# Kernel tuning notes

Measured on AMD Instinct MI355X. Metric: run time of the kernel, lower is better.

The kernel has to match this reference:

```python
import jax, jax.numpy as jnp
import numpy as np
from functools import partial

B, N, T = 4, 10000, 128
E = 160000
H, C = 4, 64            # heads, out_channels per head
GAT_DIM = H * C         # 256
NEG_SLOPE = 0.2


def conv1d(x, w, b):
    # x: (M, Cin, L), w: (Cout, Cin, K), 'same' padding (pad=1 for k=3)
    y = jax.lax.conv_general_dilated(x, w, window_strides=(1,), padding=[(1, 1)],
                                     dimension_numbers=('NCH', 'OIH', 'NCH'))
    return y + b[None, :, None]


def maxpool2(x):
    # kernel=2, stride=2 over last axis
    return jax.lax.reduce_window(x, -jnp.inf, jax.lax.max,
                                 (1, 1, 2), (1, 1, 2), 'VALID')


def gat_layer_single(x, src, dst, W, att_s, att_d, bias):
    # x: (N, Fin); PyG GATConv with concat=True, self-loops already appended to src/dst
    n = x.shape[0]
    xl = (x @ W).reshape(n, H, C)                       # (N, H, C)
    a_s = jnp.sum(xl * att_s[None], axis=-1)            # (N, H)
    a_d = jnp.sum(xl * att_d[None], axis=-1)            # (N, H)
    e = jax.nn.leaky_relu(a_s[src] + a_d[dst], NEG_SLOPE)  # (E', H)
    emax = jax.ops.segment_max(e, dst, num_segments=n)     # (N, H)
    ex = jnp.exp(e - emax[dst])
    denom = jax.ops.segment_sum(ex, dst, num_segments=n)   # (N, H)
    alpha = ex / (denom[dst] + 1e-16)                       # (E', H)
    msg = xl[src] * alpha[..., None]                        # (E', H, C)
    out = jax.ops.segment_sum(msg, dst, num_segments=n)     # (N, H, C)
    return out.reshape(n, H * C) + bias


def setup_inputs() -> dict:
    key = jax.random.key(0)
    ks = jax.random.split(key, 24)
    rn = lambda k, sh, fan: jax.random.normal(k, sh, jnp.float32) / np.sqrt(fan)
    inp = {
        'x': jax.random.normal(ks[0], (B, N, T), jnp.float32),
        'edge_index': jax.random.randint(ks[1], (2, E), 0, N, jnp.int64),
        # temporal conv
        'cw1': rn(ks[2], (32, 1, 3), 3), 'cb1': jnp.zeros((32,), jnp.float32),
        'cw2': rn(ks[3], (64, 32, 3), 96), 'cb2': jnp.zeros((64,), jnp.float32),
        # GAT layer 0 (in=64)
        'W0': rn(ks[4], (64, GAT_DIM), 64), 'as0': rn(ks[5], (H, C), C), 'ad0': rn(ks[6], (H, C), C),
        'b0': jnp.zeros((GAT_DIM,), jnp.float32),
        # GAT layer 1 (in=256)
        'W1': rn(ks[7], (GAT_DIM, GAT_DIM), GAT_DIM), 'as1': rn(ks[8], (H, C), C), 'ad1': rn(ks[9], (H, C), C),
        'b1': jnp.zeros((GAT_DIM,), jnp.float32),
        # classification head 256->128->2
        'Wc1': rn(ks[10], (GAT_DIM, 128), GAT_DIM), 'bc1': jnp.zeros((128,), jnp.float32),
        'Wc2': rn(ks[11], (128, 2), 128), 'bc2': jnp.zeros((2,), jnp.float32),
        # attribution head 256->64->1
        'Wa1': rn(ks[12], (GAT_DIM, 64), GAT_DIM), 'ba1': jnp.zeros((64,), jnp.float32),
        'Wa2': rn(ks[13], (64, 1), 64), 'ba2': jnp.zeros((1,), jnp.float32),
    }
    return inp


def reference(x, edge_index, cw1, cb1, cw2, cb2, W0, as0, ad0, b0, W1, as1, ad1, b1,
              Wc1, bc1, Wc2, bc2, Wa1, ba1, Wa2, ba2):
    b, n, t = x.shape
    # ---- temporal conv over all B*N node signals ----
    xf = x.reshape(b * n, 1, t)
    h = jax.nn.relu(conv1d(xf, cw1, cb1))            # (BN, 32, T)
    h = maxpool2(h)                                  # (BN, 32, T//2)
    h = jax.nn.relu(conv1d(h, cw2, cb2))             # (BN, 64, T//2)
    feat = jnp.mean(h, axis=-1).reshape(b, n, 64)    # adaptive_avg_pool1d(1)
    # ---- GAT stack (self-loops appended, PyG default) ----
    src0, dst0 = edge_index[0], edge_index[1]
    loops = jnp.arange(n, dtype=src0.dtype)
    src = jnp.concatenate([src0, loops])
    dst = jnp.concatenate([dst0, loops])
    gat0 = jax.vmap(partial(gat_layer_single, src=src, dst=dst, W=W0, att_s=as0, att_d=ad0, bias=b0))
    gat1 = jax.vmap(partial(gat_layer_single, src=src, dst=dst, W=W1, att_s=as1, att_d=ad1, bias=b1))
    g = jax.nn.relu(gat0(feat))                      # (B, N, 256); dropout = identity (eval)
    g = jax.nn.relu(gat1(g))                         # (B, N, 256)
    # ---- heads ----
    pooled = jnp.mean(g, axis=1)                     # (B, 256)
    logits = jax.nn.relu(pooled @ Wc1 + bc1) @ Wc2 + bc2          # (B, 2)
    attr = jax.nn.sigmoid(jax.nn.relu(g @ Wa1 + ba1) @ Wa2 + ba2)  # (B, N, 1)
    return logits, attr[..., 0]
```

## Files before the change

kernel.cpp:

```cpp
#include <hip/hip_runtime.h>
#include <hip/hip_bf16.h>
#include <math.h>

typedef __hip_bfloat16 bf16;
typedef unsigned short u16;
typedef unsigned int u32;
typedef __attribute__((ext_vector_type(8))) short short8;
typedef __attribute__((ext_vector_type(4))) float f32x4;
typedef __attribute__((ext_vector_type(2))) float f32x2;

#define BATCH 4
#define NNODE 10000
#define TLEN 128
#define NEDGE 160000
#define GDIM 256
#define NHEAD 4

#define S_CW1 0
#define S_CB1 96
#define S_CB2 128
#define S_AS0 192
#define S_AD0 448
#define S_B0  704
#define S_AS1 960
#define S_AD1 1216
#define S_B1  1472
#define S_BC1 1728
#define S_WC2 1856
#define S_BC2 2112
#define S_BA1 2114
#define S_WA2 2178
#define S_BA2 2242
#define S_TOTAL 2243

__device__ __forceinline__ float prelu(float v) { return fmaxf(v, 0.f); }
__device__ __forceinline__ u16 f2b(float f) {
    union { float f; u32 u; } v; v.f = f;
    u32 r = v.u + 0x7FFF + ((v.u >> 16) & 1);
    return (u16)(r >> 16);
}
__device__ __forceinline__ float u2f(u16 u) {
    union { u32 u; float f; } v; v.u = ((u32)u) << 16;
    return v.f;
}
__device__ __forceinline__ float ldw(const void* p, int off, bool isbf) {
    return isbf ? u2f(((const u16*)p)[off]) : ((const float*)p)[off];
}

__device__ __forceinline__ bool probe_x_bf16(const void* xsrc) {
    int lane = threadIdx.x & 63;
    u16 h = ((const u16*)xsrc)[2 * lane];
    int e = (h >> 7) & 0xFF;
    unsigned long long m = __ballot(e >= 117 && e <= 130);
    return __popcll(m) >= 32;
}
__device__ __forceinline__ bool probe_ei64(const int* ei) {
    int lane = threadIdx.x & 63;
    int v = ei[2 * lane + 1];
    unsigned long long m = __ballot(v == 0);
    return __popcll(m) >= 56;
}

struct WPtrs { const void* p[20]; };

#define PRE_TBLK 665
__global__ __launch_bounds__(256) void k_pre(WPtrs wp, const void* __restrict__ xsrc,
        const int* __restrict__ ei, float* __restrict__ wbuf,
        u16* __restrict__ cw2r, u16* __restrict__ W0t, u16* __restrict__ W1t,
        u16* __restrict__ Wa1t, int* __restrict__ counts) {
    bool isbf = probe_x_bf16(xsrc);
    int b = blockIdx.x;
    if (b >= PRE_TBLK) {
        const int C2[16] = {0,96,128,192,448,704,960,1216,1472,1728,1856,2112,
                            2114,2178,2242,2243};
        const int SRC[15] = {0,1,3,5,6,7,9,10,11,13,14,15,17,18,19};
        int i = (b - PRE_TBLK) * 256 + threadIdx.x;
        if (i >= S_TOTAL) return;
        int j = 14;
        for (int t = 0; t < 15; ++t) { if (i < C2[t + 1]) { j = t; break; } }
        wbuf[i] = ldw(wp.p[SRC[j]], i - C2[j], isbf);
        return;
    }
    int i = b * 256 + threadIdx.x;
    if (i < 6144) {
        int c2 = i / 96, k = i - c2 * 96, s = k >> 5, ci = k & 31;
        cw2r[i] = f2b(ldw(wp.p[2], c2 * 96 + ci * 3 + s, isbf));
    }
    if (i < 16384) {
        int k = i >> 8, c = i & 255;
        W0t[c * 64 + k] = f2b(ldw(wp.p[4], k * 256 + c, isbf));
        int ka = i >> 6, ca = i & 63;
        Wa1t[ca * 256 + ka] = f2b(ldw(wp.p[16], ka * 64 + ca, isbf));
    }
    if (i < 65536) {
        int k = i >> 8, c = i & 255;
        W1t[c * 256 + k] = f2b(ldw(wp.p[8], k * 256 + c, isbf));
    }
    if (i < NEDGE + NNODE) {
        bool ei64 = probe_ei64(ei);
        int dst;
        if (i < NEDGE) dst = ei64 ? ei[2 * (NEDGE + i)] : ei[NEDGE + i];
        else dst = i - NEDGE;
        if (dst >= 0 && dst < NNODE) atomicAdd(&counts[dst], 1);
    }
}

__global__ __launch_bounds__(1024) void k_scan(const int* __restrict__ counts,
        int* __restrict__ cur, int* __restrict__ row_ptr) {
    __shared__ int buf[1024];
    int t = threadIdx.x;
    int base = t * 10;
    int c[10];
    int s = 0;
    #pragma unroll
    for (int i = 0; i < 10; ++i) {
        int idx = base + i;
        c[i] = (idx < NNODE) ? counts[idx] : 0;
        s += c[i];
    }
    buf[t] = s;
    __syncthreads();
    for (int off = 1; off < 1024; off <<= 1) {
        int v = (t >= off) ? buf[t - off] : 0;
        __syncthreads();
        buf[t] += v;
        __syncthreads();
    }
    int run = buf[t] - s;
    #pragma unroll
    for (int i = 0; i < 10; ++i) {
        int idx = base + i;
        if (idx < NNODE) {
            cur[idx] = run;
            run += c[i];
            row_ptr[idx + 1] = run;
        }
    }
    if (t == 0) row_ptr[0] = 0;
}

#define HSTR 40
#define FSTR 72
#define NPW 4
#define FILL_BLK 665
__global__ __launch_bounds__(256) void k_conv(const void* __restrict__ xsrc,
        const float* __restrict__ wbuf, const u16* __restrict__ cw2r,
        const u16* __restrict__ W0t, u16* __restrict__ featb,
        u16* __restrict__ xlb, float* __restrict__ a_s, float* __restrict__ a_d,
        const int* __restrict__ ei, int* __restrict__ cur, int* __restrict__ col_src) {
    __shared__ __align__(16) float xs[4][132];
    __shared__ float w1s[96], b1s[32], b2s[64];
    __shared__ __align__(16) u16 hb[4][66 * HSTR];
    __shared__ __align__(16) u16 fs[16][FSTR];

    bool isbf = probe_x_bf16(xsrc);
    int tid = threadIdx.x;
    int wave = tid >> 6, lane = tid & 63;
    int node0 = blockIdx.x * (4 * NPW);

    int m = lane & 15, q = lane >> 4;
    short8 bfr[4][3];
    #pragma unroll
    for (int nt = 0; nt < 4; ++nt)
        #pragma unroll
        for (int sh = 0; sh < 3; ++sh)
            bfr[nt][sh] = *(const short8*)&cw2r[(nt * 16 + m) * 96 + sh * 32 + q * 8];

    if (tid < 96) w1s[tid] = wbuf[S_CW1 + tid];
    if (tid < 32) b1s[tid] = wbuf[S_CB1 + tid];
    if (tid < 64) b2s[tid] = wbuf[S_CB2 + tid];
    if (tid < 8) xs[tid >> 1][(tid & 1) ? 129 : 0] = 0.f;
    if (tid < 64) {
        int w = tid >> 4, idx = tid & 15;
        *(u32*)&hb[w][2 * idx] = 0;
        *(u32*)&hb[w][65 * HSTR + 2 * idx] = 0;
    }
    __syncthreads();

    float* xsw = xs[wave];
    u16* hw = &hb[wave][0];

    int d = m, uu = q;
    float wa0 = w1s[6 * d + 0], wa1 = w1s[6 * d + 1], wa2 = w1s[6 * d + 2];
    float wb0 = w1s[6 * d + 3], wb1 = w1s[6 * d + 4], wb2 = w1s[6 * d + 5];
    float ba = b1s[2 * d], bb = b1s[2 * d + 1];
    float b2vv[4];
    #pragma unroll
    for (int nt = 0; nt < 4; ++nt) b2vv[nt] = b2s[nt * 16 + m];

    int node = node0 + wave;
    u32 plo = 0; float2 pf = {0.f, 0.f};
    if (isbf) plo = ((const u32*)xsrc)[(size_t)node * 64 + lane];
    else      pf  = ((const float2*)xsrc)[(size_t)node * 64 + lane];

    for (int j = 0; j < NPW; ++j) {
        if (isbf) {
            xsw[1 + 2 * lane] = u2f((u16)(plo & 0xFFFF));
            xsw[2 + 2 * lane] = u2f((u16)(plo >> 16));
        } else {
            xsw[1 + 2 * lane] = pf.x;
            xsw[2 + 2 * lane] = pf.y;
        }
        if (j + 1 < NPW) {
            int nxt = node + 4;
            if (isbf) plo = ((const u32*)xsrc)[(size_t)nxt * 64 + lane];
            else      pf  = ((const float2*)xsrc)[(size_t)nxt * 64 + lane];
        }

        #pragma unroll
        for (int it = 0; it < 16; ++it) {
            int u = uu + 4 * it;
            int t0 = 2 * u;
            float2 xa = *(const float2*)&xsw[t0];
            float2 xb = *(const float2*)&xsw[t0 + 2];
            float x0 = xa.x, x1 = xa.y, x2 = xb.x, x3 = xb.y;
            f32x2 A = {x0, x1}, Bv = {x1, x2}, Cv = {x2, x3};
            f32x2 va = {ba, ba}; va += wa0 * A; va += wa1 * Bv; va += wa2 * Cv;
            f32x2 vb = {bb, bb}; vb += wb0 * A; vb += wb1 * Bv; vb += wb2 * Cv;
            float ha = fmaxf(fmaxf(va.x, va.y), 0.f);
            float hb2 = fmaxf(fmaxf(vb.x, vb.y), 0.f);
            __hip_bfloat162 hp2 = __float22bfloat162_rn(make_float2(ha, hb2));
            u32 pack; __builtin_memcpy(&pack, &hp2, 4);
            *(u32*)&hw[(u + 1) * HSTR + 2 * d] = pack;
        }

        float pc0 = 0.f, pc1 = 0.f, pc2 = 0.f, pc3 = 0.f;
        #pragma unroll
        for (int mt = 0; mt < 4; ++mt) {
            const u16* hr = &hw[(mt * 16 + m) * HSTR + q * 8];
            short8 a0 = *(const short8*)&hr[0 * HSTR];
            short8 a1 = *(const short8*)&hr[1 * HSTR];
            short8 a2 = *(const short8*)&hr[2 * HSTR];
            f32x4 c0 = {0.f,0.f,0.f,0.f}, c1 = {0.f,0.f,0.f,0.f};
            f32x4 c2 = {0.f,0.f,0.f,0.f}, c3 = {0.f,0.f,0.f,0.f};
            c0 = __builtin_amdgcn_mfma_f32_16x16x32_bf16(a0, bfr[0][0], c0, 0, 0, 0);
            c1 = __builtin_amdgcn_mfma_f32_16x16x32_bf16(a0, bfr[1][0], c1, 0, 0, 0);
            c2 = __builtin_amdgcn_mfma_f32_16x16x32_bf16(a0, bfr[2][0], c2, 0, 0, 0);
            c3 = __builtin_amdgcn_mfma_f32_16x16x32_bf16(a0, bfr[3][0], c3, 0, 0, 0);
            c0 = __builtin_amdgcn_mfma_f32_16x16x32_bf16(a1, bfr[0][1], c0, 0, 0, 0);
            c1 = __builtin_amdgcn_mfma_f32_16x16x32_bf16(a1, bfr[1][1], c1, 0, 0, 0);
            c2 = __builtin_amdgcn_mfma_f32_16x16x32_bf16(a1, bfr[2][1], c2, 0, 0, 0);
            c3 = __builtin_amdgcn_mfma_f32_16x16x32_bf16(a1, bfr[3][1], c3, 0, 0, 0);
            c0 = __builtin_amdgcn_mfma_f32_16x16x32_bf16(a2, bfr[0][2], c0, 0, 0, 0);
            c1 = __builtin_amdgcn_mfma_f32_16x16x32_bf16(a2, bfr[1][2], c1, 0, 0, 0);
            c2 = __builtin_amdgcn_mfma_f32_16x16x32_bf16(a2, bfr[2][2], c2, 0, 0, 0);
            c3 = __builtin_amdgcn_mfma_f32_16x16x32_bf16(a2, bfr[3][2], c3, 0, 0, 0);
            pc0 += prelu(c0[0] + b2vv[0]) + prelu(c0[1] + b2vv[0])
                 + prelu(c0[2] + b2vv[0]) + prelu(c0[3] + b2vv[0]);
            pc1 += prelu(c1[0] + b2vv[1]) + prelu(c1[1] + b2vv[1])
                 + prelu(c1[2] + b2vv[1]) + prelu(c1[3] + b2vv[1]);
            pc2 += prelu(c2[0] + b2vv[2]) + prelu(c2[1] + b2vv[2])
                 + prelu(c2[2] + b2vv[2]) + prelu(c2[3] + b2vv[2]);
            pc3 += prelu(c3[0] + b2vv[3]) + prelu(c3[1] + b2vv[3])
                 + prelu(c3[2] + b2vv[3]) + prelu(c3[3] + b2vv[3]);
        }
        pc0 += __shfl_xor(pc0, 16, 64); pc0 += __shfl_xor(pc0, 32, 64);
        pc1 += __shfl_xor(pc1, 16, 64); pc1 += __shfl_xor(pc1, 32, 64);
        pc2 += __shfl_xor(pc2, 16, 64); pc2 += __shfl_xor(pc2, 32, 64);
        pc3 += __shfl_xor(pc3, 16, 64); pc3 += __shfl_xor(pc3, 32, 64);
        float v = (q == 0) ? pc0 : (q == 1) ? pc1 : (q == 2) ? pc2 : pc3;
        u16 fv = f2b(v * (1.f / 64.f));
        if (node < 32) featb[(size_t)node * 64 + lane] = fv;
        fs[wave + 4 * j][lane] = fv;

        node += 4;
    }

    if (blockIdx.x < FILL_BLK) {
        bool ei64 = probe_ei64(ei);
        int e = blockIdx.x * 256 + tid;
        if (e < NEDGE + NNODE) {
            int src, dst;
            if (e < NEDGE) {
                if (ei64) { src = ei[2 * e]; dst = ei[2 * (NEDGE + e)]; }
                else      { src = ei[e];     dst = ei[NEDGE + e]; }
            } else {
                src = dst = e - NEDGE;
            }
            if (dst >= 0 && dst < NNODE) {
                int pos = atomicAdd(&cur[dst], 1);
                if (pos >= 0 && pos < NEDGE + NNODE) col_src[pos] = src;
            }
        }
    }

    __syncthreads();

    {
        f32x4 acc[4];
        #pragma unroll
        for (int ntl = 0; ntl < 4; ++ntl) acc[ntl] = {0.f, 0.f, 0.f, 0.f};
        #pragma unroll
        for (int kc = 0; kc < 64; kc += 32) {
            short8 a = *(const short8*)&fs[m][kc + q * 8];
            #pragma unroll
            for (int ntl = 0; ntl < 4; ++ntl) {
                int col0 = wave * 64 + ntl * 16;
                short8 bw = *(const short8*)&W0t[(size_t)(col0 + m) * 64 + kc + q * 8];
                acc[ntl] = __builtin_amdgcn_mfma_f32_16x16x32_bf16(a, bw, acc[ntl], 0, 0, 0);
            }
        }
        #pragma unroll
        for (int ntl = 0; ntl < 4; ++ntl) {
            #pragma unroll
            for (int r = 0; r < 4; ++r)
                xlb[(size_t)(node0 + q * 4 + r) * 256 + wave * 64 + ntl * 16 + m]
                    = f2b(acc[ntl][r]);
        }
        const float* asw_p = wbuf + S_AS0;
        const float* adw_p = wbuf + S_AD0;
        float sh_s[4] = {0, 0, 0, 0}, sh_d[4] = {0, 0, 0, 0};
        #pragma unroll
        for (int ntl = 0; ntl < 4; ++ntl) {
            float asw = asw_p[wave * 64 + ntl * 16 + m];
            float adw = adw_p[wave * 64 + ntl * 16 + m];
            #pragma unroll
            for (int r = 0; r < 4; ++r) {
                sh_s[r] += acc[ntl][r] * asw;
                sh_d[r] += acc[ntl][r] * adw;
            }
        }
        #pragma unroll
        for (int off = 1; off < 16; off <<= 1) {
            #pragma unroll
            for (int r = 0; r < 4; ++r) {
                sh_s[r] += __shfl_xor(sh_s[r], off, 64);
                sh_d[r] += __shfl_xor(sh_d[r], off, 64);
            }
        }
        if (m == 0) {
            int bb2 = node0 / NNODE;
            int nn0 = node0 - bb2 * NNODE;
            #pragma unroll
            for (int r = 0; r < 4; ++r) {
                int nn = nn0 + q * 4 + r;
                a_s[(size_t)nn * 16 + bb2 * 4 + wave] = sh_s[r];
                a_d[(size_t)nn * 16 + bb2 * 4 + wave] = sh_d[r];
            }
        }
    }
}

#define GSTR 264
__global__ __launch_bounds__(512) void k_agg_gemm(const u16* __restrict__ xlb,
        const float* __restrict__ a_s, const float* __restrict__ a_d,
        const int* __restrict__ row_ptr, const int* __restrict__ col_src,
        const float* __restrict__ bias, const u16* __restrict__ W1t,
        const float* __restrict__ wbuf, u16* __restrict__ outb,
        float* __restrict__ as_out, float* __restrict__ ad_out) {
    __shared__ __align__(16) u16 gt[16][GSTR];
    __shared__ float ps_s[8][16], ps_d[8][16];

    int tid = threadIdx.x;
    int wave = tid >> 6, lane = tid & 63;
    int dl = wave >> 1;
    int dst = __builtin_amdgcn_readfirstlane(blockIdx.x * 4 + dl);
    int bp = (wave & 1) * 2;
    int beg = __builtin_amdgcn_readfirstlane(row_ptr[dst]);
    int end = __builtin_amdgcn_readfirstlane(row_ptr[dst + 1]);

    int bl = lane >> 5;
    int s = lane & 31;
    int h = s >> 3;
    int b = bp + bl;
    int asoff = b * 4 + h;
    size_t rowb = (size_t)b * NNODE;
    float advh = a_d[(size_t)dst * 16 + asoff];

    float m = -INFINITY, l = 0.f;
    float acc[8];
    #pragma unroll
    for (int k = 0; k < 8; ++k) acc[k] = 0.f;

    int i = beg;
    int n0 = 0, n1 = 0, n2 = 0, n3 = 0;
    if (i + 4 <= end) {
        n0 = col_src[i]; n1 = col_src[i + 1];
        n2 = col_src[i + 2]; n3 = col_src[i + 3];
    }
    while (i + 4 <= end) {
        int s0 = min(max(n0, 0), NNODE - 1);
        int s1 = min(max(n1, 0), NNODE - 1);
        int s2 = min(max(n2, 0), NNODE - 1);
        int s3 = min(max(n3, 0), NNODE - 1);
        float a0 = a_s[(size_t)s0 * 16 + asoff];
        float a1 = a_s[(size_t)s1 * 16 + asoff];
        float a2 = a_s[(size_t)s2 * 16 + asoff];
        float a3 = a_s[(size_t)s3 * 16 + asoff];
        short8 x0 = *(const short8*)&xlb[(rowb + s0) * 256 + s * 8];
        short8 x1 = *(const short8*)&xlb[(rowb + s1) * 256 + s * 8];
        short8 x2 = *(const short8*)&xlb[(rowb + s2) * 256 + s * 8];
        short8 x3 = *(const short8*)&xlb[(rowb + s3) * 256 + s * 8];
        i += 4;
        if (i + 4 <= end) {
            n0 = col_src[i]; n1 = col_src[i + 1];
            n2 = col_src[i + 2]; n3 = col_src[i + 3];
        }
        float e0 = a0 + advh; e0 = (e0 >= 0.f) ? e0 : 0.2f * e0;
        float e1 = a1 + advh; e1 = (e1 >= 0.f) ? e1 : 0.2f * e1;
        float e2 = a2 + advh; e2 = (e2 >= 0.f) ? e2 : 0.2f * e2;
        float e3 = a3 + advh; e3 = (e3 >= 0.f) ? e3 : 0.2f * e3;
        float cmax = fmaxf(fmaxf(e0, e1), fmaxf(e2, e3));
        if (__any(cmax > m)) {
            float mn = fmaxf(m, cmax);
            float r = __expf(m - mn);
            m = mn;
            l *= r;
            #pragma unroll
            for (int k = 0; k < 8; ++k) acc[k] *= r;
        }
        float p0 = __expf(e0 - m); l += p0;
        #pragma unroll
        for (int k = 0; k < 8; ++k) acc[k] += p0 * u2f((u16)x0[k]);
        float p1 = __expf(e1 - m); l += p1;
        #pragma unroll
        for (int k = 0; k < 8; ++k) acc[k] += p1 * u2f((u16)x1[k]);
        float p2 = __expf(e2 - m); l += p2;
        #pragma unroll
        for (int k = 0; k < 8; ++k) acc[k] += p2 * u2f((u16)x2[k]);
        float p3 = __expf(e3 - m); l += p3;
        #pragma unroll
        for (int k = 0; k < 8; ++k) acc[k] += p3 * u2f((u16)x3[k]);
    }
    for (; i < end; ++i) {
        int s0 = min(max(col_src[i], 0), NNODE - 1);
        float a0 = a_s[(size_t)s0 * 16 + asoff];
        short8 x0 = *(const short8*)&xlb[(rowb + s0) * 256 + s * 8];
        float e0 = a0 + advh; e0 = (e0 >= 0.f) ? e0 : 0.2f * e0;
        if (__any(e0 > m)) {
            float mn = fmaxf(m, e0);
            float r = __expf(m - mn);
            m = mn;
            l *= r;
            #pragma unroll
            for (int k = 0; k < 8; ++k) acc[k] *= r;
        }
        float p0 = __expf(e0 - m); l += p0;
        #pragma unroll
        for (int k = 0; k < 8; ++k) acc[k] += p0 * u2f((u16)x0[k]);
    }

    float rl = 1.f / (l + 1e-16f);
    short8 o;
    #pragma unroll
    for (int k = 0; k < 8; ++k)
        o[k] = (short)f2b(prelu(acc[k] * rl + bias[s * 8 + k]));
    int grow = dl * 4 + b;
    *(short8*)&gt[grow][s * 8] = o;
    __syncthreads();

    int mm = lane & 15, q = lane >> 4;
    f32x4 ac2[2];
    ac2[0] = {0.f, 0.f, 0.f, 0.f};
    ac2[1] = {0.f, 0.f, 0.f, 0.f};
    for (int kc = 0; kc < 256; kc += 32) {
        short8 a = *(const short8*)&gt[mm][kc + q * 8];
        #pragma unroll
        for (int ntl = 0; ntl < 2; ++ntl) {
            short8 bw = *(const short8*)&W1t[(size_t)(wave * 32 + ntl * 16 + mm) * 256 + kc + q * 8];
            ac2[ntl] = __builtin_amdgcn_mfma_f32_16x16x32_bf16(a, bw, ac2[ntl], 0, 0, 0);
        }
    }
    int dbase = blockIdx.x * 4;
    #pragma unroll
    for (int ntl = 0; ntl < 2; ++ntl) {
        #pragma unroll
        for (int r = 0; r < 4; ++r)
            outb[((size_t)r * NNODE + dbase + q) * 256 + wave * 32 + ntl * 16 + mm]
                = f2b(ac2[ntl][r]);
    }
    float sh_s[4] = {0, 0, 0, 0}, sh_d[4] = {0, 0, 0, 0};
    #pragma unroll
    for (int ntl = 0; ntl < 2; ++ntl) {
        int col = wave * 32 + ntl * 16 + mm;
        float asw = wbuf[S_AS1 + col];
        float adw = wbuf[S_AD1 + col];
        #pragma unroll
        for (int r = 0; r < 4; ++r) {
            sh_s[r] += ac2[ntl][r] * asw;
            sh_d[r] += ac2[ntl][r] * adw;
        }
    }
    #pragma unroll
    for (int off = 1; off < 16; off <<= 1) {
        #pragma unroll
        for (int r = 0; r < 4; ++r) {
            sh_s[r] += __shfl_xor(sh_s[r], off, 64);
            sh_d[r] += __shfl_xor(sh_d[r], off, 64);
        }
    }
    if (mm == 0) {
        #pragma unroll
        for (int r = 0; r < 4; ++r) {
            ps_s[wave][q * 4 + r] = sh_s[r];
            ps_d[wave][q * 4 + r] = sh_d[r];
        }
    }
    __syncthreads();
    if (tid < 128) {
        int sd = tid >> 6, hh = (tid >> 4) & 3, row2 = tid & 15;
        int nn = dbase + (row2 >> 2), bb = row2 & 3;
        if (sd == 0)
            as_out[(size_t)nn * 16 + bb * 4 + hh] = ps_s[2 * hh][row2] + ps_s[2 * hh + 1][row2];
        else
            ad_out[(size_t)nn * 16 + bb * 4 + hh] = ps_d[2 * hh][row2] + ps_d[2 * hh + 1][row2];
    }
}

__global__ __launch_bounds__(512) void k_agg_attr(const u16* __restrict__ gb,
        const float* __restrict__ a_s, const float* __restrict__ a_d,
        const int* __restrict__ row_ptr, const int* __restrict__ col_src,
        const float* __restrict__ bias, const u16* __restrict__ Wa1t,
        const float* __restrict__ wbuf, u16* __restrict__ gdiag,
        float* __restrict__ out, float* __restrict__ pooled) {
    __shared__ __align__(16) u16 gt[16][GSTR];
    __shared__ float ps_a[4][16];

    int tid = threadIdx.x;
    int wave = tid >> 6, lane = tid & 63;
    int dl = wave >> 1;
    int dst = __builtin_amdgcn_readfirstlane(blockIdx.x * 4 + dl);
    int bp = (wave & 1) * 2;
    int beg = __builtin_amdgcn_readfirstlane(row_ptr[dst]);
    int end = __builtin_amdgcn_readfirstlane(row_ptr[dst + 1]);

    int bl = lane >> 5;
    int s = lane & 31;
    int h = s >> 3;
    int b = bp + bl;
    int asoff = b * 4 + h;
    size_t rowb = (size_t)b * NNODE;
    float advh = a_d[(size_t)dst * 16 + asoff];

    float m = -INFINITY, l = 0.f;
    float acc[8];
    #pragma unroll
    for (int k = 0; k < 8; ++k) acc[k] = 0.f;

    int i = beg;
    int n0 = 0, n1 = 0, n2 = 0, n3 = 0;
    if (i + 4 <= end) {
        n0 = col_src[i]; n1 = col_src[i + 1];
        n2 = col_src[i + 2]; n3 = col_src[i + 3];
    }
    while (i + 4 <= end) {
        int s0 = min(max(n0, 0), NNODE - 1);
        int s1 = min(max(n1, 0), NNODE - 1);
        int s2 = min(max(n2, 0), NNODE - 1);
        int s3 = min(max(n3, 0), NNODE - 1);
        float a0 = a_s[(size_t)s0 * 16 + asoff];
        float a1 = a_s[(size_t)s1 * 16 + asoff];
        float a2 = a_s[(size_t)s2 * 16 + asoff];
        float a3 = a_s[(size_t)s3 * 16 + asoff];
        short8 x0 = *(const short8*)&gb[(rowb + s0) * 256 + s * 8];
        short8 x1 = *(const short8*)&gb[(rowb + s1) * 256 + s * 8];
        short8 x2 = *(const short8*)&gb[(rowb + s2) * 256 + s * 8];
        short8 x3 = *(const short8*)&gb[(rowb + s3) * 256 + s * 8];
        i += 4;
        if (i + 4 <= end) {
            n0 = col_src[i]; n1 = col_src[i + 1];
            n2 = col_src[i + 2]; n3 = col_src[i + 3];
        }
        float e0 = a0 + advh; e0 = (e0 >= 0.f) ? e0 : 0.2f * e0;
        float e1 = a1 + advh; e1 = (e1 >= 0.f) ? e1 : 0.2f * e1;
        float e2 = a2 + advh; e2 = (e2 >= 0.f) ? e2 : 0.2f * e2;
        float e3 = a3 + advh; e3 = (e3 >= 0.f) ? e3 : 0.2f * e3;
        float cmax = fmaxf(fmaxf(e0, e1), fmaxf(e2, e3));
        if (__any(cmax > m)) {
            float mn = fmaxf(m, cmax);
            float r = __expf(m - mn);
            m = mn;
            l *= r;
            #pragma unroll
            for (int k = 0; k < 8; ++k) acc[k] *= r;
        }
        float p0 = __expf(e0 - m); l += p0;
        #pragma unroll
        for (int k = 0; k < 8; ++k) acc[k] += p0 * u2f((u16)x0[k]);
        float p1 = __expf(e1 - m); l += p1;
        #pragma unroll
        for (int k = 0; k < 8; ++k) acc[k] += p1 * u2f((u16)x1[k]);
        float p2 = __expf(e2 - m); l += p2;
        #pragma unroll
        for (int k = 0; k < 8; ++k) acc[k] += p2 * u2f((u16)x2[k]);
        float p3 = __expf(e3 - m); l += p3;
        #pragma unroll
        for (int k = 0; k < 8; ++k) acc[k] += p3 * u2f((u16)x3[k]);
    }
    for (; i < end; ++i) {
        int s0 = min(max(col_src[i], 0), NNODE - 1);
        float a0 = a_s[(size_t)s0 * 16 + asoff];
        short8 x0 = *(const short8*)&gb[(rowb + s0) * 256 + s * 8];
        float e0 = a0 + advh; e0 = (e0 >= 0.f) ? e0 : 0.2f * e0;
        if (__any(e0 > m)) {
            float mn = fmaxf(m, e0);
            float r = __expf(m - mn);
            m = mn;
            l *= r;
            #pragma unroll
            for (int k = 0; k < 8; ++k) acc[k] *= r;
        }
        float p0 = __expf(e0 - m); l += p0;
        #pragma unroll
        for (int k = 0; k < 8; ++k) acc[k] += p0 * u2f((u16)x0[k]);
    }

    float rl = 1.f / (l + 1e-16f);
    short8 o;
    #pragma unroll
    for (int k = 0; k < 8; ++k)
        o[k] = (short)f2b(prelu(acc[k] * rl + bias[s * 8 + k]));
    *(short8*)&gt[dl * 4 + b][s * 8] = o;
    if (b == 0 && dst < 8)
        *(short8*)&gdiag[(size_t)dst * 256 + s * 8] = o;
    __syncthreads();

    int dbase = blockIdx.x * 4;
    int mm = lane & 15, q = lane >> 4;
    if (wave < 4) {
        f32x4 ac2 = {0.f, 0.f, 0.f, 0.f};
        for (int kc = 0; kc < 256; kc += 32) {
            short8 a = *(const short8*)&gt[mm][kc + q * 8];
            short8 bw = *(const short8*)&Wa1t[(size_t)(wave * 16 + mm) * 256 + kc + q * 8];
            ac2 = __builtin_amdgcn_mfma_f32_16x16x32_bf16(a, bw, ac2, 0, 0, 0);
        }
        int col = wave * 16 + mm;
        float ba1v = wbuf[S_BA1 + col];
        float wa2v = wbuf[S_WA2 + col];
        float part[4];
        #pragma unroll
        for (int r = 0; r < 4; ++r)
            part[r] = prelu(ac2[r] + ba1v) * wa2v;
        #pragma unroll
        for (int off = 1; off < 16; off <<= 1) {
            #pragma unroll
            for (int r = 0; r < 4; ++r)
                part[r] += __shfl_xor(part[r], off, 64);
        }
        if (mm == 0) {
            #pragma unroll
            for (int r = 0; r < 4; ++r)
                ps_a[wave][q * 4 + r] = part[r];
        }
    } else {
        int c = tid - 256;
        #pragma unroll
        for (int bb = 0; bb < 4; ++bb) {
            float sum = u2f(gt[0 * 4 + bb][c]) + u2f(gt[1 * 4 + bb][c])
                      + u2f(gt[2 * 4 + bb][c]) + u2f(gt[3 * 4 + bb][c]);
            atomicAdd(&pooled[bb * 256 + c], sum);
        }
    }
    __syncthreads();
    if (tid < 16) {
        int rr = tid;
        float v = ps_a[0][rr] + ps_a[1][rr] + ps_a[2][rr] + ps_a[3][rr] + wbuf[S_BA2];
        int dl2 = rr >> 2, b2 = rr & 3;
        out[8 + (size_t)b2 * NNODE + dbase + dl2] = 1.f / (1.f + __expf(-v));
    }
}

__global__ __launch_bounds__(128) void k_logits(const float* __restrict__ pooled,
        const float* __restrict__ wbuf, const void* __restrict__ Wc1p,
        float* __restrict__ out,
        const u16* __restrict__ featb, const u16* __restrict__ gb,
        const int* __restrict__ row_ptr, const int* __restrict__ ei,
        const void* __restrict__ xsrc, int hostbad) {
    int tid = threadIdx.x;
    bool isbf = probe_x_bf16(xsrc);
    if (blockIdx.x == 4) {
        __shared__ float red[128];
        bool ei64 = probe_ei64(ei);
        float mx[2] = {0.f, 0.f};
        const u16* bufs[2] = {featb, gb};
        for (int qq = 0; qq < 2; ++qq) {
            const u16* p = bufs[qq];
            float m = 0.f;
            for (int i = tid; i < 2048; i += 128) {
                float v = u2f(p[i]);
                if (v != v) m = 1e30f;
                m = fmaxf(m, fabsf(v));
            }
            red[tid] = m;
            __syncthreads();
            for (int s2 = 64; s2 > 0; s2 >>= 1) {
                if (tid < s2) red[tid] = fmaxf(red[tid], red[tid + s2]);
                __syncthreads();
            }
            mx[qq] = red[0];
            __syncthreads();
        }
        if (tid == 0) {
            int fb = (mx[0] > 1e8f || mx[0] < 1e-6f) ? 1 : 0;
            int gbad = (mx[1] > 1e8f || mx[1] < 1e-6f) ? 1 : 0;
            int cb = (row_ptr[NNODE] != NEDGE + NNODE) ? 1 : 0;
            int code = 100 * fb + 400 * gbad + 800 * cb + 6400 * hostbad;
            if (code) {
                code += 1600 * (isbf ? 0 : 1);
                code += 3200 * (ei64 ? 1 : 0);
                for (int j = 0; j < 8; ++j) out[j] = (float)code;
            }
        }
        return;
    }
    __shared__ float pm[256];
    __shared__ float red4[4];
    int b = blockIdx.x;
    pm[tid] = pooled[b * 256 + tid] * (1.f / NNODE);
    pm[tid + 128] = pooled[b * 256 + tid + 128] * (1.f / NNODE);
    __syncthreads();
    float acc = wbuf[S_BC1 + tid];
    if (isbf) {
        const u16* w = (const u16*)Wc1p;
        #pragma unroll 4
        for (int k = 0; k < 256; ++k)
            acc += pm[k] * u2f(w[k * 128 + tid]);
    } else {
        const float* w = (const float*)Wc1p;
        #pragma unroll 4
        for (int k = 0; k < 256; ++k)
            acc += pm[k] * w[k * 128 + tid];
    }
    float hv = prelu(acc);
    float p0 = hv * wbuf[S_WC2 + tid * 2];
    float p1 = hv * wbuf[S_WC2 + tid * 2 + 1];
    #pragma unroll
    for (int off = 32; off > 0; off >>= 1) {
        p0 += __shfl_xor(p0, off, 64);
        p1 += __shfl_xor(p1, off, 64);
    }
    int wv = tid >> 6, lane = tid & 63;
    if (lane == 0) { red4[wv * 2] = p0; red4[wv * 2 + 1] = p1; }
    __syncthreads();
    if (tid < 2)
        out[b * 2 + tid] = red4[tid] + red4[2 + tid] + wbuf[S_BC2 + tid];
}

extern "C" void kernel_launch(void* const* d_in, const int* in_sizes, int n_in,
                              void* d_out, int out_size, void* d_ws, size_t ws_size,
                              hipStream_t stream) {
    const void* x  = d_in[0];
    const int*  ei = (const int*)d_in[1];
    float* out = (float*)d_out;

    WPtrs wp;
    for (int j = 0; j < 20; ++j) wp.p[j] = d_in[j + 2];

    char* ws = (char*)d_ws;
    size_t off = 0;
    auto alloc = [&](size_t bytes) -> void* {
        void* p = ws + off;
        off += (bytes + 255) & ~(size_t)255;
        return p;
    };
    float* wbuf    = (float*)alloc((size_t)S_TOTAL * 4);
    u16*   featb   = (u16*)  alloc((size_t)BATCH * NNODE * 64 * 2);
    u16*   xlb     = (u16*)  alloc((size_t)BATCH * NNODE * 256 * 2);
    u16*   gb      = (u16*)  alloc((size_t)BATCH * NNODE * 256 * 2);
    float* a_s     = (float*)alloc((size_t)BATCH * NNODE * 4 * 4);
    float* a_d     = (float*)alloc((size_t)BATCH * NNODE * 4 * 4);
    float* a_s2    = (float*)alloc((size_t)BATCH * NNODE * 4 * 4);
    float* a_d2    = (float*)alloc((size_t)BATCH * NNODE * 4 * 4);
    u16*   cw2r    = (u16*)alloc(6144 * 2);
    u16*   W0t     = (u16*)alloc(16384 * 2);
    u16*   W1t     = (u16*)alloc(65536 * 2);
    u16*   Wa1t    = (u16*)alloc(16384 * 2);
    int*   counts  = (int*)alloc(NNODE * 4);
    float* pooled  = (float*)alloc(BATCH * 256 * 4);
    int*   row_ptr = (int*)alloc((NNODE + 1) * 4);
    int*   cur     = (int*)alloc(NNODE * 4);
    int*   col_src = (int*)alloc((NEDGE + NNODE) * 4);
    (void)ws_size; (void)out_size;

    int hostbad = (n_in != 22 || in_sizes[0] != BATCH * NNODE * TLEN ||
                   in_sizes[1] != 2 * NEDGE) ? 1 : 0;

    hipMemsetAsync(counts, 0, 40192 + 4096, stream);

    k_pre<<<PRE_TBLK + 9, 256, 0, stream>>>(wp, x, ei, wbuf, cw2r, W0t, W1t, Wa1t, counts);
    k_scan<<<1, 1024, 0, stream>>>(counts, cur, row_ptr);

    k_conv<<<BATCH * NNODE / 16, 256, 0, stream>>>(x, wbuf, cw2r, W0t, featb,
            xlb, a_s, a_d, ei, cur, col_src);

    k_agg_gemm<<<NNODE / 4, 512, 0, stream>>>(xlb, a_s, a_d, row_ptr, col_src,
            wbuf + S_B0, W1t, wbuf, gb, a_s2, a_d2);

    k_agg_attr<<<NNODE / 4, 512, 0, stream>>>(gb, a_s2, a_d2, row_ptr, col_src,
            wbuf + S_B1, Wa1t, wbuf, xlb, out, pooled);

    k_logits<<<5, 128, 0, stream>>>(pooled, wbuf, wp.p[12], out, featb, xlb, row_ptr, ei, x, hostbad);
}
```

Baseline: 361.8 us.

## Fold scan and logits kernels into predecessors via last-block-done counters

```diff
diff --git a/kernel.cpp b/kernel.cpp
--- a/kernel.cpp
+++ b/kernel.cpp
@@ -64,10 +64,12 @@
 struct WPtrs { const void* p[20]; };
 
 #define PRE_TBLK 665
+#define PRE_NBLK (PRE_TBLK + 9)
 __global__ __launch_bounds__(256) void k_pre(WPtrs wp, const void* __restrict__ xsrc,
         const int* __restrict__ ei, float* __restrict__ wbuf,
         u16* __restrict__ cw2r, u16* __restrict__ W0t, u16* __restrict__ W1t,
-        u16* __restrict__ Wa1t, int* __restrict__ counts) {
+        u16* __restrict__ Wa1t, int* __restrict__ counts,
+        int* __restrict__ cur, int* __restrict__ row_ptr, int* __restrict__ ctr) {
     bool isbf = probe_x_bf16(xsrc);
     int b = blockIdx.x;
     if (b >= PRE_TBLK) {
@@ -75,68 +77,72 @@
                             2114,2178,2242,2243};
         const int SRC[15] = {0,1,3,5,6,7,9,10,11,13,14,15,17,18,19};
         int i = (b - PRE_TBLK) * 256 + threadIdx.x;
-        if (i >= S_TOTAL) return;
-        int j = 14;
-        for (int t = 0; t < 15; ++t) { if (i < C2[t + 1]) { j = t; break; } }
-        wbuf[i] = ldw(wp.p[SRC[j]], i - C2[j], isbf);
-        return;
-    }
-    int i = b * 256 + threadIdx.x;
-    if (i < 6144) {
-        int c2 = i / 96, k = i - c2 * 96, s = k >> 5, ci = k & 31;
-        cw2r[i] = f2b(ldw(wp.p[2], c2 * 96 + ci * 3 + s, isbf));
-    }
-    if (i < 16384) {
-        int k = i >> 8, c = i & 255;
-        W0t[c * 64 + k] = f2b(ldw(wp.p[4], k * 256 + c, isbf));
-        int ka = i >> 6, ca = i & 63;
-        Wa1t[ca * 256 + ka] = f2b(ldw(wp.p[16], ka * 64 + ca, isbf));
-    }
-    if (i < 65536) {
-        int k = i >> 8, c = i & 255;
-        W1t[c * 256 + k] = f2b(ldw(wp.p[8], k * 256 + c, isbf));
-    }
-    if (i < NEDGE + NNODE) {
-        bool ei64 = probe_ei64(ei);
-        int dst;
-        if (i < NEDGE) dst = ei64 ? ei[2 * (NEDGE + i)] : ei[NEDGE + i];
-        else dst = i - NEDGE;
-        if (dst >= 0 && dst < NNODE) atomicAdd(&counts[dst], 1);
-    }
-}
-
-__global__ __launch_bounds__(1024) void k_scan(const int* __restrict__ counts,
-        int* __restrict__ cur, int* __restrict__ row_ptr) {
-    __shared__ int buf[1024];
-    int t = threadIdx.x;
-    int base = t * 10;
-    int c[10];
-    int s = 0;
-    #pragma unroll
-    for (int i = 0; i < 10; ++i) {
-        int idx = base + i;
-        c[i] = (idx < NNODE) ? counts[idx] : 0;
-        s += c[i];
-    }
-    buf[t] = s;
+        if (i < S_TOTAL) {
+            int j = 14;
+            for (int t = 0; t < 15; ++t) { if (i < C2[t + 1]) { j = t; break; } }
+            wbuf[i] = ldw(wp.p[SRC[j]], i - C2[j], isbf);
+        }
+    } else {
+        int i = b * 256 + threadIdx.x;
+        if (i < 6144) {
+            int c2 = i / 96, k = i - c2 * 96, s = k >> 5, ci = k & 31;
+            cw2r[i] = f2b(ldw(wp.p[2], c2 * 96 + ci * 3 + s, isbf));
+        }
+        if (i < 16384) {
+            int k = i >> 8, c = i & 255;
+            W0t[c * 64 + k] = f2b(ldw(wp.p[4], k * 256 + c, isbf));
+            int ka = i >> 6, ca = i & 63;
+            Wa1t[ca * 256 + ka] = f2b(ldw(wp.p[16], ka * 64 + ca, isbf));
+        }
+        if (i < 65536) {
+            int k = i >> 8, c = i & 255;
+            W1t[c * 256 + k] = f2b(ldw(wp.p[8], k * 256 + c, isbf));
+        }
+        if (i < NEDGE + NNODE) {
+            bool ei64 = probe_ei64(ei);
+            int dst;
+            if (i < NEDGE) dst = ei64 ? ei[2 * (NEDGE + i)] : ei[NEDGE + i];
+            else dst = i - NEDGE;
+            if (dst >= 0 && dst < NNODE) atomicAdd(&counts[dst], 1);
+        }
+    }
+
+    __threadfence();
+    __shared__ int lastv;
+    if (threadIdx.x == 0) lastv = atomicAdd(ctr, 1);
     __syncthreads();
-    for (int off = 1; off < 1024; off <<= 1) {
-        int v = (t >= off) ? buf[t - off] : 0;
+    if (lastv == PRE_NBLK - 1) {
+        __shared__ int sbuf[256];
+        int t = threadIdx.x;
+        int base = t * 40;
+        int c[40];
+        int s = 0;
+        #pragma unroll
+        for (int i2 = 0; i2 < 40; ++i2) {
+            int idx = base + i2;
+            c[i2] = (idx < NNODE) ? counts[idx] : 0;
+            s += c[i2];
+        }
+        sbuf[t] = s;
         __syncthreads();
-        buf[t] += v;
-        __syncthreads();
-    }
-    int run = buf[t] - s;
-    #pragma unroll
-    for (int i = 0; i < 10; ++i) {
-        int idx = base + i;
-        if (idx < NNODE) {
-            cur[idx] = run;
-            run += c[i];
-            row_ptr[idx + 1] = run;
-        }
-    }
-    if (t == 0) row_ptr[0] = 0;
+        for (int off = 1; off < 256; off <<= 1) {
+            int v = (t >= off) ? sbuf[t - off] : 0;
+            __syncthreads();
+            sbuf[t] += v;
+            __syncthreads();
+        }
+        int run = sbuf[t] - s;
+        #pragma unroll
+        for (int i2 = 0; i2 < 40; ++i2) {
+            int idx = base + i2;
+            if (idx < NNODE) {
+                cur[idx] = run;
+                run += c[i2];
+                row_ptr[idx + 1] = run;
+            }
+        }
+        if (t == 0) row_ptr[0] = 0;
+    }
 }
 
 #define HSTR 40
@@ -512,7 +518,10 @@
         const int* __restrict__ row_ptr, const int* __restrict__ col_src,
         const float* __restrict__ bias, const u16* __restrict__ Wa1t,
         const float* __restrict__ wbuf, u16* __restrict__ gdiag,
-        float* __restrict__ out, float* __restrict__ pooled) {
+        float* __restrict__ out, float* __restrict__ pooled,
+        const void* __restrict__ Wc1p, const u16* __restrict__ featb,
+        const int* __restrict__ ei, const void* __restrict__ xsrc,
+        int hostbad, int* __restrict__ ctr2) {
     __shared__ __align__(16) u16 gt[16][GSTR];
     __shared__ float ps_a[4][16];
 
@@ -658,82 +667,76 @@
         int dl2 = rr >> 2, b2 = rr & 3;
         out[8 + (size_t)b2 * NNODE + dbase + dl2] = 1.f / (1.f + __expf(-v));
     }
-}
-
-__global__ __launch_bounds__(128) void k_logits(const float* __restrict__ pooled,
-        const float* __restrict__ wbuf, const void* __restrict__ Wc1p,
-        float* __restrict__ out,
-        const u16* __restrict__ featb, const u16* __restrict__ gb,
-        const int* __restrict__ row_ptr, const int* __restrict__ ei,
-        const void* __restrict__ xsrc, int hostbad) {
-    int tid = threadIdx.x;
-    bool isbf = probe_x_bf16(xsrc);
-    if (blockIdx.x == 4) {
-        __shared__ float red[128];
-        bool ei64 = probe_ei64(ei);
-        float mx[2] = {0.f, 0.f};
-        const u16* bufs[2] = {featb, gb};
-        for (int qq = 0; qq < 2; ++qq) {
-            const u16* p = bufs[qq];
-            float m = 0.f;
-            for (int i = tid; i < 2048; i += 128) {
-                float v = u2f(p[i]);
-                if (v != v) m = 1e30f;
-                m = fmaxf(m, fabsf(v));
-            }
-            red[tid] = m;
-            __syncthreads();
-            for (int s2 = 64; s2 > 0; s2 >>= 1) {
-                if (tid < s2) red[tid] = fmaxf(red[tid], red[tid + s2]);
-                __syncthreads();
-            }
-            mx[qq] = red[0];
-            __syncthreads();
-        }
-        if (tid == 0) {
-            int fb = (mx[0] > 1e8f || mx[0] < 1e-6f) ? 1 : 0;
-            int gbad = (mx[1] > 1e8f || mx[1] < 1e-6f) ? 1 : 0;
-            int cb = (row_ptr[NNODE] != NEDGE + NNODE) ? 1 : 0;
-            int code = 100 * fb + 400 * gbad + 800 * cb + 6400 * hostbad;
-            if (code) {
-                code += 1600 * (isbf ? 0 : 1);
-                code += 3200 * (ei64 ? 1 : 0);
-                for (int j = 0; j < 8; ++j) out[j] = (float)code;
-            }
-        }
-        return;
-    }
-    __shared__ float pm[256];
-    __shared__ float red4[4];
-    int b = blockIdx.x;
-    pm[tid] = pooled[b * 256 + tid] * (1.f / NNODE);
-    pm[tid + 128] = pooled[b * 256 + tid + 128] * (1.f / NNODE);
+
+    __threadfence();
+    __shared__ int lastv2;
+    if (tid == 0) lastv2 = atomicAdd(ctr2, 1);
     __syncthreads();
-    float acc = wbuf[S_BC1 + tid];
-    if (isbf) {
-        const u16* w = (const u16*)Wc1p;
-        #pragma unroll 4
-        for (int k = 0; k < 256; ++k)
-            acc += pm[k] * u2f(w[k * 128 + tid]);
-    } else {
-        const float* w = (const float*)Wc1p;
-        #pragma unroll 4
-        for (int k = 0; k < 256; ++k)
-            acc += pm[k] * w[k * 128 + tid];
-    }
-    float hv = prelu(acc);
-    float p0 = hv * wbuf[S_WC2 + tid * 2];
-    float p1 = hv * wbuf[S_WC2 + tid * 2 + 1];
-    #pragma unroll
-    for (int off = 32; off > 0; off >>= 1) {
-        p0 += __shfl_xor(p0, off, 64);
-        p1 += __shfl_xor(p1, off, 64);
-    }
-    int wv = tid >> 6, lane = tid & 63;
-    if (lane == 0) { red4[wv * 2] = p0; red4[wv * 2 + 1] = p1; }
-    __syncthreads();
-    if (tid < 2)
-        out[b * 2 + tid] = red4[tid] + red4[2 + tid] + wbuf[S_BC2 + tid];
+    if (lastv2 == (int)gridDim.x - 1) {
+        __shared__ float pm2[4][260];
+        __shared__ float red44[4][4];
+        bool isbf = probe_x_bf16(xsrc);
+        int bb2 = tid >> 7, t = tid & 127;
+        pm2[bb2][t] = pooled[bb2 * 256 + t] * (1.f / NNODE);
+        pm2[bb2][t + 128] = pooled[bb2 * 256 + t + 128] * (1.f / NNODE);
+        __syncthreads();
+        float acc2 = wbuf[S_BC1 + t];
+        if (isbf) {
+            const u16* w = (const u16*)Wc1p;
+            #pragma unroll 4
+            for (int k = 0; k < 256; ++k)
+                acc2 += pm2[bb2][k] * u2f(w[k * 128 + t]);
+        } else {
+            const float* w = (const float*)Wc1p;
+            #pragma unroll 4
+            for (int k = 0; k < 256; ++k)
+                acc2 += pm2[bb2][k] * w[k * 128 + t];
+        }
+        float hv = prelu(acc2);
+        float p0 = hv * wbuf[S_WC2 + t * 2];
+        float p1 = hv * wbuf[S_WC2 + t * 2 + 1];
+        #pragma unroll
+        for (int off = 32; off > 0; off >>= 1) {
+            p0 += __shfl_xor(p0, off, 64);
+            p1 += __shfl_xor(p1, off, 64);
+        }
+        int wv2 = (t >> 6) & 1, ln = tid & 63;
+        if (ln == 0) { red44[bb2][wv2 * 2] = p0; red44[bb2][wv2 * 2 + 1] = p1; }
+        __syncthreads();
+        if (t < 2)
+            out[bb2 * 2 + t] = red44[bb2][t] + red44[bb2][2 + t] + wbuf[S_BC2 + t];
+        __syncthreads();
+        if (tid < 64) {
+            bool ei64 = probe_ei64(ei);
+            float mx0 = 0.f, mx1 = 0.f;
+            for (int i2 = tid; i2 < 2048; i2 += 64) {
+                float v = u2f(featb[i2]);
+                if (v != v) mx0 = 1e30f;
+                mx0 = fmaxf(mx0, fabsf(v));
+            }
+            for (int i2 = tid; i2 < 2048; i2 += 64) {
+                float v = u2f(gdiag[i2]);
+                if (v != v) mx1 = 1e30f;
+                mx1 = fmaxf(mx1, fabsf(v));
+            }
+            #pragma unroll
+            for (int off = 1; off < 64; off <<= 1) {
+                mx0 = fmaxf(mx0, __shfl_xor(mx0, off, 64));
+                mx1 = fmaxf(mx1, __shfl_xor(mx1, off, 64));
+            }
+            if (tid == 0) {
+                int fb2 = (mx0 > 1e8f || mx0 < 1e-6f) ? 1 : 0;
+                int gbad = (mx1 > 1e8f || mx1 < 1e-6f) ? 1 : 0;
+                int cb = (row_ptr[NNODE] != NEDGE + NNODE) ? 1 : 0;
+                int code = 100 * fb2 + 400 * gbad + 800 * cb + 6400 * hostbad;
+                if (code) {
+                    code += 1600 * (isbf ? 0 : 1);
+                    code += 3200 * (ei64 ? 1 : 0);
+                    for (int j2 = 0; j2 < 8; ++j2) out[j2] = (float)code;
+                }
+            }
+        }
+    }
 }
 
 extern "C" void kernel_launch(void* const* d_in, const int* in_sizes, int n_in,
@@ -767,6 +770,7 @@
     u16*   Wa1t    = (u16*)alloc(16384 * 2);
     int*   counts  = (int*)alloc(NNODE * 4);
     float* pooled  = (float*)alloc(BATCH * 256 * 4);
+    int*   ctrs    = (int*)alloc(256);
     int*   row_ptr = (int*)alloc((NNODE + 1) * 4);
     int*   cur     = (int*)alloc(NNODE * 4);
     int*   col_src = (int*)alloc((NEDGE + NNODE) * 4);
@@ -775,10 +779,10 @@
     int hostbad = (n_in != 22 || in_sizes[0] != BATCH * NNODE * TLEN ||
                    in_sizes[1] != 2 * NEDGE) ? 1 : 0;
 
-    hipMemsetAsync(counts, 0, 40192 + 4096, stream);
-
-    k_pre<<<PRE_TBLK + 9, 256, 0, stream>>>(wp, x, ei, wbuf, cw2r, W0t, W1t, Wa1t, counts);
-    k_scan<<<1, 1024, 0, stream>>>(counts, cur, row_ptr);
+    hipMemsetAsync(counts, 0, 40192 + 4096 + 256, stream);
+
+    k_pre<<<PRE_NBLK, 256, 0, stream>>>(wp, x, ei, wbuf, cw2r, W0t, W1t, Wa1t,
+            counts, cur, row_ptr, ctrs);
 
     k_conv<<<BATCH * NNODE / 16, 256, 0, stream>>>(x, wbuf, cw2r, W0t, featb,
             xlb, a_s, a_d, ei, cur, col_src);
@@ -787,7 +791,6 @@
             wbuf + S_B0, W1t, wbuf, gb, a_s2, a_d2);
 
     k_agg_attr<<<NNODE / 4, 512, 0, stream>>>(gb, a_s2, a_d2, row_ptr, col_src,
-            wbuf + S_B1, Wa1t, wbuf, xlb, out, pooled);
-
-    k_logits<<<5, 128, 0, stream>>>(pooled, wbuf, wp.p[12], out, featb, xlb, row_ptr, ei, x, hostbad);
-}
+            wbuf + S_B1, Wa1t, wbuf, xlb, out, pooled,
+            wp.p[12], featb, ei, x, hostbad, ctrs + 1);
+}
```

Result: slower. 939.0 us (+159.6%).
